# Optimization experiments

Measured on AMD Instinct MI355X. Metric: run time of the kernel, lower is better.

## Reference

```python
import jax, jax.numpy as jnp
import numpy as np


def _ln(x, g, b, eps=1e-5):
    m = x.mean(-1, keepdims=True)
    v = ((x - m) ** 2).mean(-1, keepdims=True)
    return (x - m) / jnp.sqrt(v + eps) * g + b


def _gat_layer(x, src, dst, W, a_src, a_dst, bias, heads, out_ch, concat):
    # PyG GATConv: linear -> per-edge leaky_relu attention -> segment softmax over dst -> scatter-sum
    N = x.shape[0]
    h = (x @ W).reshape(N, heads, out_ch)            # [N,H,C]
    asrc = (h * a_src).sum(-1)                        # [N,H]
    adst = (h * a_dst).sum(-1)                        # [N,H]
    e = jax.nn.leaky_relu(asrc[src] + adst[dst], 0.2)  # [E,H]
    m = jax.ops.segment_max(e, dst, num_segments=N)
    p = jnp.exp(e - m[dst])
    denom = jax.ops.segment_sum(p, dst, num_segments=N)
    alpha = p / (denom[dst] + 1e-16)                  # [E,H]
    out = jax.ops.segment_sum(h[src] * alpha[:, :, None], dst, num_segments=N)  # [N,H,C]
    out = out.reshape(N, heads * out_ch) if concat else out.mean(1)
    return out + bias


def setup_inputs() -> dict:
    k = jax.random.key(0)
    def rn(i, shape, s=0.05):
        return jax.random.normal(jax.random.fold_in(k, i), shape, dtype=jnp.float32) * s
    N, E, B, S = 50000, 800000, 8, 512
    return dict(
        hidden_states=rn(0, (B, S, 768), 1.0),
        attention_mask=jnp.ones((B, S), jnp.int32),
        concept_embeddings_bert=rn(1, (111, 768), 1.0),
        graph_x=rn(2, (N, 256), 1.0),
        edge_index=jax.random.randint(jax.random.fold_in(k, 3), (2, E), 0, N),
        concept_node_idx=jax.random.randint(jax.random.fold_in(k, 4), (111,), 0, N),
        w1=rn(5, (256, 256)), att_src1=rn(6, (4, 64)), att_dst1=rn(7, (4, 64)), bias1=rn(8, (256,)),
        w2=rn(9, (256, 256)), att_src2=rn(10, (1, 256)), att_dst2=rn(11, (1, 256)), bias2=rn(12, (256,)),
        graph_proj_w=rn(13, (768, 256)), graph_proj_b=rn(14, (768,)),
        fusion_w=rn(15, (768, 1536)), fusion_b=rn(16, (768,)),
        fusion_ln_g=jnp.ones((768,), jnp.float32), fusion_ln_b=jnp.zeros((768,), jnp.float32),
        in_proj_w=rn(17, (2304, 768)), in_proj_b=rn(18, (2304,)),
        out_proj_w=rn(19, (768, 768)), out_proj_b=rn(20, (768,)),
        ln_g=jnp.ones((768,), jnp.float32), ln_b=jnp.zeros((768,), jnp.float32),
        concept_head_w=rn(21, (111, 768)), concept_head_b=rn(22, (111,)),
        laat_first_w=rn(23, (768, 768)), laat_second_w=rn(24, (50, 768)),
        laat_output_w=rn(25, (1, 768)), laat_output_b=rn(26, (1,)),
        c2l_w=rn(27, (50, 111)),
        graph_scale=jnp.array([-2.0], jnp.float32),
    )


def reference(hidden_states, attention_mask, concept_embeddings_bert, graph_x, edge_index,
              concept_node_idx, w1, att_src1, att_dst1, bias1, w2, att_src2, att_dst2, bias2,
              graph_proj_w, graph_proj_b, fusion_w, fusion_b, fusion_ln_g, fusion_ln_b,
              in_proj_w, in_proj_b, out_proj_w, out_proj_b, ln_g, ln_b,
              concept_head_w, concept_head_b, laat_first_w, laat_second_w,
              laat_output_w, laat_output_b, c2l_w, graph_scale):
    N = graph_x.shape[0]
    B, S, H = hidden_states.shape
    loop = jnp.arange(N, dtype=edge_index.dtype)  # PyG add_self_loops default
    src = jnp.concatenate([edge_index[0], loop])
    dst = jnp.concatenate([edge_index[1], loop])
    # --- GATEncoder (2 layers, eval mode => dropout identity) ---
    g = _gat_layer(graph_x, src, dst, w1, att_src1, att_dst1, bias1, 4, 64, True)
    g = jax.nn.elu(g)
    g = _gat_layer(g, src, dst, w2, att_src2, att_dst2, bias2, 1, 256, False)  # [N,256]
    gat_concepts = g[concept_node_idx] @ graph_proj_w.T + graph_proj_b          # [NC,768]
    # --- concept fusion ---
    NC = concept_embeddings_bert.shape[0]
    fused_in = jnp.concatenate([
        jnp.broadcast_to(concept_embeddings_bert, (B, NC, H)),
        jnp.broadcast_to(gat_concepts, (B, NC, H))], axis=-1)                   # [B,NC,1536]
    enhanced = jax.nn.relu(_ln(fused_in @ fusion_w.T + fusion_b, fusion_ln_g, fusion_ln_b))
    # --- cross attention (8 heads, dim 96) ---
    wq, wk, wv = in_proj_w[:768], in_proj_w[768:1536], in_proj_w[1536:]
    bq, bk, bv = in_proj_b[:768], in_proj_b[768:1536], in_proj_b[1536:]
    q = (hidden_states @ wq.T + bq).reshape(B, S, 8, 96)
    kk = (enhanced @ wk.T + bk).reshape(B, NC, 8, 96)
    vv = (enhanced @ wv.T + bv).reshape(B, NC, 8, 96)
    scores = jnp.einsum('bshd,bchd->bhsc', q, kk) / jnp.sqrt(jnp.float32(96.0))
    attn = jax.nn.softmax(scores, axis=-1)                                      # [B,8,S,NC]
    ctx = jnp.einsum('bhsc,bchd->bshd', attn, vv).reshape(B, S, H)
    context = ctx @ out_proj_w.T + out_proj_b
    attn_weights = attn.mean(1)                                                 # [B,S,NC]
    # --- concept head on CLS ---
    concept_logits = hidden_states[:, 0] @ concept_head_w.T + concept_head_b
    concept_scores = jax.nn.sigmoid(concept_logits)
    graph_strength = jax.nn.sigmoid(graph_scale[0])
    enriched = _ln(hidden_states + graph_strength * context, ln_g, ln_b)
    # --- LAAT ---
    U = jnp.tanh(enriched @ laat_first_w.T)
    att = U @ laat_second_w.T                                                   # [B,S,ND]
    att = jnp.where(attention_mask[:, :, None] == 0, -jnp.inf, att)
    w = jax.nn.softmax(att, axis=1)
    label_reps = jnp.einsum('bsl,bsh->blh', w, enriched)                        # [B,ND,H]
    logits = (label_reps @ laat_output_w.T)[..., 0] + laat_output_b[0]
    logits = logits + concept_scores @ c2l_w.T
    return (logits, concept_logits, concept_scores, label_reps, attn_weights, graph_strength)
```

## Files before the change

### kernel.cpp

```cpp
#include <hip/hip_runtime.h>
#include <math.h>
#include <stdint.h>

static constexpr int NN = 50000;
static constexpr int EE = 800000;
static constexpr int ET = EE + NN;
static constexpr int BB = 8;
static constexpr int SS = 512;
static constexpr int HH = 768;
static constexpr int NC = 111;
static constexpr int NL = 50;

#define DINL __device__ __forceinline__

typedef __attribute__((ext_vector_type(8))) short bf16x8;
typedef __attribute__((ext_vector_type(4))) float f32x4;

DINL float wsum(float v){
  #pragma unroll
  for (int m=1;m<64;m<<=1) v += __shfl_xor(v, m);
  return v;
}
DINL float wmax(float v){
  #pragma unroll
  for (int m=1;m<64;m<<=1) v = fmaxf(v, __shfl_xor(v, m));
  return v;
}
DINL float4 wsum4(float4 v){
  #pragma unroll
  for (int m=1;m<64;m<<=1){
    v.x += __shfl_xor(v.x,m); v.y += __shfl_xor(v.y,m);
    v.z += __shfl_xor(v.z,m); v.w += __shfl_xor(v.w,m);
  }
  return v;
}
DINL float4 wmax4(float4 v){
  #pragma unroll
  for (int m=1;m<64;m<<=1){
    v.x=fmaxf(v.x,__shfl_xor(v.x,m)); v.y=fmaxf(v.y,__shfl_xor(v.y,m));
    v.z=fmaxf(v.z,__shfl_xor(v.z,m)); v.w=fmaxf(v.w,__shfl_xor(v.w,m));
  }
  return v;
}

__global__ void count_deg_k(const int* __restrict__ eidx, int* __restrict__ deg){
  int i = blockIdx.x*256 + threadIdx.x;
  if (i>=ET) return;
  int d = (i<EE)? eidx[EE + i] : (i - EE);
  atomicAdd(&deg[d], 1);
}

__global__ __launch_bounds__(1024) void scan1_k(const int* __restrict__ deg,
                                                int* __restrict__ incl, int* __restrict__ csum){
  __shared__ int sh[1024];
  int tid = threadIdx.x;
  int i = blockIdx.x*1024 + tid;
  int v = (i<NN)? deg[i] : 0;
  sh[tid] = v;
  __syncthreads();
  for (int off=1; off<1024; off<<=1){
    int t = (tid>=off)? sh[tid-off] : 0;
    __syncthreads();
    sh[tid] += t;
    __syncthreads();
  }
  if (i<NN) incl[i] = sh[tid];
  if (tid==1023) csum[blockIdx.x] = sh[1023];
}

__global__ void scan2_k(int* __restrict__ csum, int nch){
  if (threadIdx.x==0 && blockIdx.x==0){
    int run = 0;
    for (int i=0;i<nch;i++){ int v = csum[i]; csum[i] = run; run += v; }
  }
}

__global__ void scan3_k(const int* __restrict__ deg, const int* __restrict__ incl,
                        const int* __restrict__ csum, int* __restrict__ rowstart){
  int i = blockIdx.x*256 + threadIdx.x;
  if (i>=NN) return;
  int ex = csum[i>>10] + incl[i] - deg[i];
  rowstart[i] = ex;
  if (i==NN-1) rowstart[NN] = ex + deg[i];
}

__global__ void fill_csr_k(const int* __restrict__ eidx, const int* __restrict__ rowstart,
                           int* __restrict__ cursor, int* __restrict__ csr_src, int* __restrict__ csr_dst){
  int i = blockIdx.x*256 + threadIdx.x;
  if (i>=ET) return;
  int s, d;
  if (i<EE){ s = eidx[i]; d = eidx[EE+i]; } else { s = i-EE; d = i-EE; }
  int pos = rowstart[d] + atomicAdd(&cursor[d], 1);
  csr_src[pos] = s; csr_dst[pos] = d;
}

DINL uint bf16_rne(float x){
  uint u = __float_as_uint(x);
  return (u + 0x7FFFu + ((u>>16)&1u)) >> 16;
}
DINL void split8(const float4 v0, const float4 v1, uint4& ph, uint4& pl){
  float xs[8] = {v0.x,v0.y,v0.z,v0.w,v1.x,v1.y,v1.z,v1.w};
  uint hh[8], ll[8];
  #pragma unroll
  for (int i=0;i<8;i++){
    uint hb = bf16_rne(xs[i]);
    float hf = __uint_as_float(hb<<16);
    float lo = xs[i] - hf;
    hh[i] = hb; ll[i] = bf16_rne(lo);
  }
  ph = make_uint4(hh[0]|(hh[1]<<16), hh[2]|(hh[3]<<16), hh[4]|(hh[5]<<16), hh[6]|(hh[7]<<16));
  pl = make_uint4(ll[0]|(ll[1]<<16), ll[2]|(ll[3]<<16), ll[4]|(ll[5]<<16), ll[6]|(ll[7]<<16));
}

__global__ void split_k(const float* __restrict__ in, ushort* __restrict__ hi,
                        ushort* __restrict__ lo, int n){
  int i = blockIdx.x*256 + threadIdx.x;
  if (i>=n) return;
  float x = in[i];
  uint hb = bf16_rne(x);
  float hf = __uint_as_float(hb<<16);
  hi[i] = (ushort)hb;
  lo[i] = (ushort)bf16_rne(x - hf);
}

__global__ void split_t_k(const float* __restrict__ in, ushort* __restrict__ hi,
                          ushort* __restrict__ lo, int R, int C){
  int i = blockIdx.x*256 + threadIdx.x;
  if (i>=R*C) return;
  int n = i / R, k = i - n*R;
  float x = in[k*C + n];
  uint hb = bf16_rne(x);
  float hf = __uint_as_float(hb<<16);
  hi[i] = (ushort)hb;
  lo[i] = (ushort)bf16_rne(x - hf);
}

__global__ __launch_bounds__(256) void gemm_mfma3(
    const float* __restrict__ A, const ushort* __restrict__ Bh, const ushort* __restrict__ Bl,
    const float* __restrict__ bias, float* __restrict__ C, ushort* __restrict__ Cb,
    int M, int N, int K, float alpha, int act)
{
  __shared__ __align__(16) ushort As[2][128*64];
  __shared__ __align__(16) ushort Bs[2][64*64];
  const int tid = threadIdx.x;
  const int lane = tid & 63, wid = tid >> 6;
  const int wm = wid >> 1, wn = wid & 1;
  const int m0 = blockIdx.y*128, n0 = blockIdx.x*64;
  f32x4 acc[4][2];
  #pragma unroll
  for (int i=0;i<4;i++)
    #pragma unroll
    for (int j=0;j<2;j++) acc[i][j] = (f32x4){0.f,0.f,0.f,0.f};

  const int nkt = K >> 6;
  for (int kt=0; kt<nkt; ++kt){
    #pragma unroll
    for (int q=0;q<4;q++){
      int idx = q*256 + tid;
      int row = idx >> 3;
      int g8  = idx & 7;
      int rowg = m0 + row; if (rowg >= M) rowg = M-1;
      const float* src = A + (int64_t)rowg*K + (kt<<6) + g8*8;
      float4 v0 = ((const float4*)src)[0];
      float4 v1 = ((const float4*)src)[1];
      uint4 ph, pl;
      split8(v0, v1, ph, pl);
      int off = row*64 + ((g8*8) ^ ((row&7)<<3));
      *(uint4*)&As[0][off] = ph;
      *(uint4*)&As[1][off] = pl;
    }
    #pragma unroll
    for (int q=0;q<4;q++){
      int idx = q*256 + tid;
      int plane = idx >> 9;
      int rem = idx & 511;
      int row = rem >> 3;
      int g8 = rem & 7;
      const ushort* src = (plane ? Bl : Bh) + (int64_t)(n0+row)*K + (kt<<6) + g8*8;
      uint4 v = *(const uint4*)src;
      int off = row*64 + ((g8*8) ^ ((row&7)<<3));
      *(uint4*)&Bs[plane][off] = v;
    }
    __syncthreads();
    #pragma unroll
    for (int ks=0; ks<2; ks++){
      const int kswz = ks*32 + ((lane>>4)<<3);
      bf16x8 ah[4], al[4], bh[2], bl[2];
      #pragma unroll
      for (int mi=0;mi<4;mi++){
        int r = wm*64 + mi*16 + (lane&15);
        int off = r*64 + (kswz ^ ((r&7)<<3));
        ah[mi] = *(const bf16x8*)&As[0][off];
        al[mi] = *(const bf16x8*)&As[1][off];
      }
      #pragma unroll
      for (int nj=0;nj<2;nj++){
        int r = wn*32 + nj*16 + (lane&15);
        int off = r*64 + (kswz ^ ((r&7)<<3));
        bh[nj] = *(const bf16x8*)&Bs[0][off];
        bl[nj] = *(const bf16x8*)&Bs[1][off];
      }
      #pragma unroll
      for (int mi=0;mi<4;mi++)
        #pragma unroll
        for (int nj=0;nj<2;nj++){
          acc[mi][nj] = __builtin_amdgcn_mfma_f32_16x16x32_bf16(ah[mi], bh[nj], acc[mi][nj], 0,0,0);
          acc[mi][nj] = __builtin_amdgcn_mfma_f32_16x16x32_bf16(ah[mi], bl[nj], acc[mi][nj], 0,0,0);
          acc[mi][nj] = __builtin_amdgcn_mfma_f32_16x16x32_bf16(al[mi], bh[nj], acc[mi][nj], 0,0,0);
        }
    }
    __syncthreads();
  }
  const int crow = (lane>>4)*4, ccol = lane&15;
  #pragma unroll
  for (int nj=0;nj<2;nj++){
    int n = n0 + wn*32 + nj*16 + ccol;
    float bv = bias ? bias[n] : 0.f;
    #pragma unroll
    for (int mi=0;mi<4;mi++){
      #pragma unroll
      for (int j=0;j<4;j++){
        int m = m0 + wm*64 + mi*16 + crow + j;
        if (m < M){
          float v = acc[mi][nj][j]*alpha + bv;
          if (act==1) v = tanhf(v);
          C[(int64_t)m*N + n] = v;
          if (Cb) Cb[(int64_t)m*N + n] = (ushort)bf16_rne(v);
        }
      }
    }
  }
}

template<bool TB>
__global__ __launch_bounds__(256) void gemm_f32(
    const float* __restrict__ A, const float* __restrict__ Bm,
    const float* __restrict__ bias, float* __restrict__ C,
    int M, int N, int K, int lda, int ldb, int ldc,
    int nb2,
    int64_t sA1, int64_t sA2, int64_t sB1, int64_t sB2, int64_t sC1, int64_t sC2,
    float alpha, int act)
{
  int z = blockIdx.z;
  int z1 = z / nb2, z2 = z - z1*nb2;
  A  += z1*sA1 + z2*sA2;
  Bm += z1*sB1 + z2*sB2;
  C  += z1*sC1 + z2*sC2;
  __shared__ __align__(16) float sA[16][132];
  __shared__ __align__(16) float sB[16][68];
  const int tid = threadIdx.x;
  const int m0 = blockIdx.y*128, n0 = blockIdx.x*64;
  const int tx = tid & 15, ty = tid >> 4;
  float acc[8][4] = {};
  for (int k0=0; k0<K; k0+=16){
    {
      int kk = tid & 15, mm = tid >> 4;
      #pragma unroll
      for (int r=0;r<8;r++){
        int m = m0 + mm + r*16, k = k0 + kk;
        float v = 0.f;
        if (m<M && k<K) v = A[(int64_t)m*lda + k];
        sA[kk][mm + r*16] = v;
      }
    }
    if (!TB){
      int nn = tid & 63, kb = tid >> 6;
      #pragma unroll
      for (int r=0;r<4;r++){
        int k = k0 + kb + r*4, n = n0 + nn;
        float v=0.f;
        if (k<K && n<N) v = Bm[(int64_t)k*ldb + n];
        sB[kb + r*4][nn] = v;
      }
    } else {
      int kk = tid & 15, nn = tid >> 4;
      #pragma unroll
      for (int r=0;r<4;r++){
        int n = n0 + nn + r*16, k = k0 + kk;
        float v=0.f;
        if (n<N && k<K) v = Bm[(int64_t)n*ldb + k];
        sB[kk][nn + r*16] = v;
      }
    }
    __syncthreads();
    #pragma unroll
    for (int k=0;k<16;k++){
      float4 a0 = *(const float4*)&sA[k][ty*8];
      float4 a1 = *(const float4*)&sA[k][ty*8+4];
      float4 b  = *(const float4*)&sB[k][tx*4];
      float av[8] = {a0.x,a0.y,a0.z,a0.w,a1.x,a1.y,a1.z,a1.w};
      float bv[4] = {b.x,b.y,b.z,b.w};
      #pragma unroll
      for (int i=0;i<8;i++)
        #pragma unroll
        for (int j=0;j<4;j++)
          acc[i][j] += av[i]*bv[j];
    }
    __syncthreads();
  }
  #pragma unroll
  for (int i=0;i<8;i++){
    int m = m0 + ty*8 + i;
    if (m>=M) continue;
    #pragma unroll
    for (int j=0;j<4;j++){
      int n = n0 + tx*4 + j;
      if (n>=N) continue;
      float v = acc[i][j]*alpha;
      if (bias) v += bias[n];
      if (act==1) v = tanhf(v);
      C[(int64_t)m*ldc + n] = v;
    }
  }
}

__global__ __launch_bounds__(256) void skinny_tb_k(
    const float* __restrict__ A, const float* __restrict__ B,
    const float* __restrict__ bias, float* __restrict__ C,
    int M, int N, int K, int lda, int ldb, int ldc)
{
  int ngroups = (N+3)>>2;
  int w = blockIdx.x*4 + (threadIdx.x>>6);
  if (w >= M*ngroups) return;
  int lane = threadIdx.x & 63;
  int m = w / ngroups, ng = w - m*ngroups;
  int n0 = ng*4;
  const float4* a4 = (const float4*)(A + (int64_t)m*lda);
  int r0 = n0, r1 = (n0+1<N)? n0+1 : N-1, r2 = (n0+2<N)? n0+2 : N-1, r3 = (n0+3<N)? n0+3 : N-1;
  const float4* b0 = (const float4*)(B + (int64_t)r0*ldb);
  const float4* b1 = (const float4*)(B + (int64_t)r1*ldb);
  const float4* b2 = (const float4*)(B + (int64_t)r2*ldb);
  const float4* b3 = (const float4*)(B + (int64_t)r3*ldb);
  float4 acc = make_float4(0.f,0.f,0.f,0.f);
  int K4 = K>>2;
  for (int i=lane; i<K4; i+=64){
    float4 av = a4[i];
    float4 v0 = b0[i], v1 = b1[i], v2 = b2[i], v3 = b3[i];
    acc.x += av.x*v0.x + av.y*v0.y + av.z*v0.z + av.w*v0.w;
    acc.y += av.x*v1.x + av.y*v1.y + av.z*v1.z + av.w*v1.w;
    acc.z += av.x*v2.x + av.y*v2.y + av.z*v2.z + av.w*v2.w;
    acc.w += av.x*v3.x + av.y*v3.y + av.z*v3.z + av.w*v3.w;
  }
  acc = wsum4(acc);
  if (lane==0){
    float vals[4] = {acc.x, acc.y, acc.z, acc.w};
    #pragma unroll
    for (int j=0;j<4;j++){
      int n = n0+j;
      if (n<N){
        float v = vals[j];
        if (bias) v += bias[n];
        C[(int64_t)m*ldc + n] = v;
      }
    }
  }
}

__global__ __launch_bounds__(256) void attcoef1_k(const float* __restrict__ h,
    const float* __restrict__ a_src, const float* __restrict__ a_dst,
    float* __restrict__ asrc, float* __restrict__ adst){
  int node = blockIdx.x*4 + (threadIdx.x>>6);
  if (node>=NN) return;
  int lane = threadIdx.x & 63;
  float4 hv = ((const float4*)h)[(int64_t)node*64 + lane];
  int head = lane >> 4;
  float4 as = ((const float4*)a_src)[head*16 + (lane&15)];
  float4 ad = ((const float4*)a_dst)[head*16 + (lane&15)];
  float ps = hv.x*as.x + hv.y*as.y + hv.z*as.z + hv.w*as.w;
  float pd = hv.x*ad.x + hv.y*ad.y + hv.z*ad.z + hv.w*ad.w;
  #pragma unroll
  for (int m=1;m<16;m<<=1){ ps += __shfl_xor(ps,m); pd += __shfl_xor(pd,m); }
  if ((lane&15)==0){ asrc[node*4+head]=ps; adst[node*4+head]=pd; }
}

__global__ __launch_bounds__(256) void attcoef2_k(const float* __restrict__ h,
    const float* __restrict__ a_src, const float* __restrict__ a_dst,
    float* __restrict__ asrc, float* __restrict__ adst){
  int node = blockIdx.x*4 + (threadIdx.x>>6);
  if (node>=NN) return;
  int lane = threadIdx.x & 63;
  float4 hv = ((const float4*)h)[(int64_t)node*64 + lane];
  float4 as = ((const float4*)a_src)[lane];
  float4 ad = ((const float4*)a_dst)[lane];
  float ps = hv.x*as.x + hv.y*as.y + hv.z*as.z + hv.w*as.w;
  float pd = hv.x*ad.x + hv.y*ad.y + hv.z*ad.z + hv.w*ad.w;
  ps = wsum(ps); pd = wsum(pd);
  if (lane==0){ asrc[node]=ps; adst[node]=pd; }
}

__global__ void edge_e1_k(const int* __restrict__ csr_src, const int* __restrict__ csr_dst,
                          const float* __restrict__ asrc, const float* __restrict__ adst,
                          float* __restrict__ ebuf){
  int p = blockIdx.x*256 + threadIdx.x;
  if (p>=ET) return;
  int s = csr_src[p], d = csr_dst[p];
  float4 a = ((const float4*)asrc)[s];
  float4 b = ((const float4*)adst)[d];
  float4 e;
  e.x = a.x+b.x; e.x = (e.x>=0.f)? e.x : 0.2f*e.x;
  e.y = a.y+b.y; e.y = (e.y>=0.f)? e.y : 0.2f*e.y;
  e.z = a.z+b.z; e.z = (e.z>=0.f)? e.z : 0.2f*e.z;
  e.w = a.w+b.w; e.w = (e.w>=0.f)? e.w : 0.2f*e.w;
  ((float4*)ebuf)[p] = e;
}

__global__ void edge_e2_k(const int* __restrict__ csr_src, const int* __restrict__ csr_dst,
                          const float* __restrict__ asrc, const float* __restrict__ adst,
                          float* __restrict__ ebuf){
  int p = blockIdx.x*256 + threadIdx.x;
  if (p>=ET) return;
  int s = csr_src[p], d = csr_dst[p];
  float e = asrc[s] + adst[d];
  e = (e>=0.f)? e : 0.2f*e;
  ebuf[p] = e;
}

__global__ __launch_bounds__(256) void agg1_k(const ushort* __restrict__ hb, const float* __restrict__ ebuf,
    const int* __restrict__ rowstart, const int* __restrict__ csr_src,
    const float* __restrict__ bias, float* __restrict__ outp){
  int node = blockIdx.x*4 + (threadIdx.x>>6);
  if (node>=NN) return;
  int lane = threadIdx.x & 63;
  int rs = rowstart[node], re = rowstart[node+1];
  const float4* e4 = (const float4*)ebuf;
  float4 mx = make_float4(-INFINITY,-INFINITY,-INFINITY,-INFINITY);
  for (int p=rs+lane; p<re; p+=64){
    float4 e = e4[p];
    mx.x=fmaxf(mx.x,e.x); mx.y=fmaxf(mx.y,e.y); mx.z=fmaxf(mx.z,e.z); mx.w=fmaxf(mx.w,e.w);
  }
  mx = wmax4(mx);
  float4 sm = make_float4(0.f,0.f,0.f,0.f);
  for (int p=rs+lane; p<re; p+=64){
    float4 e = e4[p];
    sm.x += expf(e.x-mx.x); sm.y += expf(e.y-mx.y);
    sm.z += expf(e.z-mx.z); sm.w += expf(e.w-mx.w);
  }
  sm = wsum4(sm);
  int head = lane>>4;
  float m_h = head==0?mx.x:head==1?mx.y:head==2?mx.z:mx.w;
  float s_h = head==0?sm.x:head==1?sm.y:head==2?sm.z:sm.w;
  float dinv = 1.f/(s_h+1e-16f);
  const ushort4* h4 = (const ushort4*)hb;
  float4 acc = make_float4(0.f,0.f,0.f,0.f);
  for (int p=rs; p<re; ++p){
    int s = csr_src[p];
    float w = expf(ebuf[p*4+head]-m_h)*dinv;
    ushort4 hu = h4[(int64_t)s*64 + lane];
    acc.x += w*__uint_as_float(((uint)hu.x)<<16);
    acc.y += w*__uint_as_float(((uint)hu.y)<<16);
    acc.z += w*__uint_as_float(((uint)hu.z)<<16);
    acc.w += w*__uint_as_float(((uint)hu.w)<<16);
  }
  float4 bb = ((const float4*)bias)[lane];
  float4 o;
  o.x = acc.x+bb.x; o.x = (o.x>0.f)? o.x : expm1f(o.x);
  o.y = acc.y+bb.y; o.y = (o.y>0.f)? o.y : expm1f(o.y);
  o.z = acc.z+bb.z; o.z = (o.z>0.f)? o.z : expm1f(o.z);
  o.w = acc.w+bb.w; o.w = (o.w>0.f)? o.w : expm1f(o.w);
  ((float4*)outp)[(int64_t)node*64 + lane] = o;
}

__global__ __launch_bounds__(256) void agg2_k(const ushort* __restrict__ hb, const float* __restrict__ ebuf,
    const int* __restrict__ rowstart, const int* __restrict__ csr_src,
    const float* __restrict__ bias, float* __restrict__ outp){
  int node = blockIdx.x*4 + (threadIdx.x>>6);
  if (node>=NN) return;
  int lane = threadIdx.x & 63;
  int rs = rowstart[node], re = rowstart[node+1];
  float mx = -INFINITY;
  for (int p=rs+lane; p<re; p+=64) mx = fmaxf(mx, ebuf[p]);
  mx = wmax(mx);
  float sm = 0.f;
  for (int p=rs+lane; p<re; p+=64) sm += expf(ebuf[p]-mx);
  sm = wsum(sm);
  float dinv = 1.f/(sm+1e-16f);
  const ushort4* h4 = (const ushort4*)hb;
  float4 acc = make_float4(0.f,0.f,0.f,0.f);
  for (int p=rs; p<re; ++p){
    int s = csr_src[p];
    float w = expf(ebuf[p]-mx)*dinv;
    ushort4 hu = h4[(int64_t)s*64 + lane];
    acc.x += w*__uint_as_float(((uint)hu.x)<<16);
    acc.y += w*__uint_as_float(((uint)hu.y)<<16);
    acc.z += w*__uint_as_float(((uint)hu.z)<<16);
    acc.w += w*__uint_as_float(((uint)hu.w)<<16);
  }
  float4 bb = ((const float4*)bias)[lane];
  float4 o = make_float4(acc.x+bb.x, acc.y+bb.y, acc.z+bb.z, acc.w+bb.w);
  ((float4*)outp)[(int64_t)node*64 + lane] = o;
}

__global__ void gather_gsel_k(const float* __restrict__ out2, const int* __restrict__ cidx,
                              float* __restrict__ gsel){
  int idx = blockIdx.x*256 + threadIdx.x;
  if (idx >= NC*256) return;
  int i = idx >> 8, c = idx & 255;
  gsel[idx] = out2[(int64_t)cidx[i]*256 + c];
}

__global__ void build_fused_k(const float* __restrict__ bert, const float* __restrict__ gatc,
                              float* __restrict__ fused){
  int idx = blockIdx.x*256 + threadIdx.x;
  if (idx >= NC*1536) return;
  int i = idx / 1536, c = idx - i*1536;
  fused[idx] = (c<768)? bert[(int64_t)i*768 + c] : gatc[(int64_t)i*768 + (c-768)];
}

__global__ __launch_bounds__(256) void ln_k(const float* __restrict__ x1, const float* __restrict__ x2,
    const float* __restrict__ gsptr, const float* __restrict__ g, const float* __restrict__ bb,
    float* __restrict__ outp, int relu){
  __shared__ float red[4];
  int row = blockIdx.x;
  int t = threadIdx.x;
  float gs = 0.f;
  if (x2) gs = 1.f/(1.f+expf(-gsptr[0]));
  const float* xr = x1 + (int64_t)row*768;
  float v0 = xr[t], v1 = xr[t+256], v2 = xr[t+512];
  if (x2){
    const float* x2r = x2 + (int64_t)row*768;
    v0 += gs*x2r[t]; v1 += gs*x2r[t+256]; v2 += gs*x2r[t+512];
  }
  int lane = t&63, wid = t>>6;
  float s = wsum(v0+v1+v2);
  if (lane==0) red[wid]=s;
  __syncthreads();
  float mean = (red[0]+red[1]+red[2]+red[3]) * (1.f/768.f);
  __syncthreads();
  float d0=v0-mean, d1=v1-mean, d2=v2-mean;
  float ss = wsum(d0*d0+d1*d1+d2*d2);
  if (lane==0) red[wid]=ss;
  __syncthreads();
  float var = (red[0]+red[1]+red[2]+red[3]) * (1.f/768.f);
  float rstd = rsqrtf(var + 1e-5f);
  float o0 = d0*rstd*g[t]+bb[t];
  float o1 = d1*rstd*g[t+256]+bb[t+256];
  float o2 = d2*rstd*g[t+512]+bb[t+512];
  if (relu){ o0=fmaxf(o0,0.f); o1=fmaxf(o1,0.f); o2=fmaxf(o2,0.f); }
  float* orow = outp + (int64_t)row*768;
  orow[t]=o0; orow[t+256]=o1; orow[t+512]=o2;
}

__global__ __launch_bounds__(256) void softmax_nc_k(float* __restrict__ sc, int rows){
  int row = blockIdx.x*4 + (threadIdx.x>>6);
  if (row>=rows) return;
  int lane = threadIdx.x & 63;
  float* r = sc + (int64_t)row*NC;
  float x0 = r[lane];
  float x1 = (lane+64<NC)? r[lane+64] : -INFINITY;
  float m = wmax(fmaxf(x0,x1));
  float p0 = expf(x0-m);
  float p1 = (lane+64<NC)? expf(x1-m) : 0.f;
  float s = wsum(p0+p1);
  float dinv = 1.f/s;
  r[lane] = p0*dinv;
  if (lane+64<NC) r[lane+64] = p1*dinv;
}

__global__ void mean_heads_k(const float* __restrict__ attn, float* __restrict__ outp){
  int64_t idx = (int64_t)blockIdx.x*256 + threadIdx.x;
  if (idx >= (int64_t)BB*SS*NC) return;
  int c = idx % NC;
  int64_t r = idx / NC;
  int s = r % SS;
  int b = r / SS;
  float acc = 0.f;
  #pragma unroll
  for (int h=0;h<8;h++)
    acc += attn[(((int64_t)(b*8+h)*SS)+s)*NC + c];
  outp[idx] = acc * 0.125f;
}

__global__ void sigmoid_k(const float* __restrict__ in, float* __restrict__ outp, int n,
                          const float* __restrict__ gsptr, float* __restrict__ gsout){
  int idx = blockIdx.x*256 + threadIdx.x;
  if (idx < n) outp[idx] = 1.f/(1.f+expf(-in[idx]));
  if (idx == 0) gsout[0] = 1.f/(1.f+expf(-gsptr[0]));
}

__global__ __launch_bounds__(256) void laat_softmax_k(float* __restrict__ att, const int* __restrict__ mask){
  int idx = blockIdx.x*4 + (threadIdx.x>>6);
  if (idx >= BB*NL) return;
  int lane = threadIdx.x & 63;
  int b = idx / NL, l = idx - b*NL;
  float x[8];
  #pragma unroll
  for (int i=0;i<8;i++){
    int s = lane + i*64;
    int mk = mask[b*SS + s];
    x[i] = mk ? att[((int64_t)(b*SS+s))*NL + l] : -INFINITY;
  }
  float m = -INFINITY;
  #pragma unroll
  for (int i=0;i<8;i++) m = fmaxf(m, x[i]);
  m = wmax(m);
  float p[8]; float sm = 0.f;
  #pragma unroll
  for (int i=0;i<8;i++){ p[i] = expf(x[i]-m); sm += p[i]; }
  sm = wsum(sm);
  float dinv = 1.f/sm;
  #pragma unroll
  for (int i=0;i<8;i++){
    int s = lane + i*64;
    att[((int64_t)(b*SS+s))*NL + l] = p[i]*dinv;
  }
}

__global__ __launch_bounds__(256) void label_reps_k(const float* __restrict__ w,
    const float* __restrict__ enr, float* __restrict__ outp){
  __shared__ __align__(16) float part[4][768];
  int bl = blockIdx.x;
  int b = bl / NL, l = bl - b*NL;
  int t = threadIdx.x;
  int wid = t>>6, lane = t&63;
  const float* wb = w + (int64_t)b*SS*NL + l;
  const float* eb = enr + (int64_t)b*SS*768;
  float4 a0 = make_float4(0,0,0,0), a1 = a0, a2 = a0;
  for (int s=wid; s<SS; s+=4){
    float wv = wb[(int64_t)s*NL];
    const float4* row = (const float4*)(eb + (int64_t)s*768);
    float4 r0 = row[lane], r1 = row[lane+64], r2 = row[lane+128];
    a0.x += wv*r0.x; a0.y += wv*r0.y; a0.z += wv*r0.z; a0.w += wv*r0.w;
    a1.x += wv*r1.x; a1.y += wv*r1.y; a1.z += wv*r1.z; a1.w += wv*r1.w;
    a2.x += wv*r2.x; a2.y += wv*r2.y; a2.z += wv*r2.z; a2.w += wv*r2.w;
  }
  ((float4*)&part[wid][lane*4      ])[0] = a0;
  ((float4*)&part[wid][lane*4 + 256])[0] = a1;
  ((float4*)&part[wid][lane*4 + 512])[0] = a2;
  __syncthreads();
  float* o = outp + (int64_t)bl*768;
  #pragma unroll
  for (int q=0;q<3;q++){
    int ch = t + q*256;
    o[ch] = part[0][ch] + part[1][ch] + part[2][ch] + part[3][ch];
  }
}

__global__ __launch_bounds__(256) void logits_k(const float* __restrict__ lr,
    const float* __restrict__ low, const float* __restrict__ lob,
    const float* __restrict__ cs, const float* __restrict__ c2l,
    float* __restrict__ logits){
  int idx = blockIdx.x*4 + (threadIdx.x>>6);
  if (idx >= BB*NL) return;
  int lane = threadIdx.x & 63;
  int b = idx / NL, l = idx - b*NL;
  const float* r = lr + (int64_t)idx*768;
  float acc = 0.f;
  for (int c=lane;c<768;c+=64) acc += r[c]*low[c];
  for (int c=lane;c<NC;c+=64)  acc += cs[b*NC+c]*c2l[l*NC+c];
  acc = wsum(acc);
  if (lane==0) logits[idx] = acc + lob[0];
}

extern "C" void kernel_launch(void* const* d_in, const int* in_sizes, int n_in,
                              void* d_out, int out_size, void* d_ws, size_t ws_size,
                              hipStream_t stream)
{
  const float* hs    = (const float*)d_in[0];
  const int*   amask = (const int*)d_in[1];
  const float* bert  = (const float*)d_in[2];
  const float* gx    = (const float*)d_in[3];
  const int*   eidx  = (const int*)d_in[4];
  const int*   cidx  = (const int*)d_in[5];
  const float* w1    = (const float*)d_in[6];
  const float* as1   = (const float*)d_in[7];
  const float* ad1   = (const float*)d_in[8];
  const float* b1    = (const float*)d_in[9];
  const float* w2    = (const float*)d_in[10];
  const float* as2   = (const float*)d_in[11];
  const float* ad2   = (const float*)d_in[12];
  const float* b2    = (const float*)d_in[13];
  const float* gpw   = (const float*)d_in[14];
  const float* gpb   = (const float*)d_in[15];
  const float* fw    = (const float*)d_in[16];
  const float* fb    = (const float*)d_in[17];
  const float* flng  = (const float*)d_in[18];
  const float* flnb  = (const float*)d_in[19];
  const float* ipw   = (const float*)d_in[20];
  const float* ipb   = (const float*)d_in[21];
  const float* opw   = (const float*)d_in[22];
  const float* opb   = (const float*)d_in[23];
  const float* lng   = (const float*)d_in[24];
  const float* lnb   = (const float*)d_in[25];
  const float* chw   = (const float*)d_in[26];
  const float* chb   = (const float*)d_in[27];
  const float* lfw   = (const float*)d_in[28];
  const float* lsw   = (const float*)d_in[29];
  const float* low   = (const float*)d_in[30];
  const float* lob   = (const float*)d_in[31];
  const float* c2l   = (const float*)d_in[32];
  const float* gsc   = (const float*)d_in[33];
  float* out = (float*)d_out;

  int* deg      = (int*)d_ws;
  int* cursor   = deg + NN;
  int* rowstart = cursor + NN;
  int* csr_src  = rowstart + (NN+1);
  int* csr_dst  = csr_src + ET;
  int* incl     = csr_dst + ET;
  int* csum     = incl + NN;
  size_t iw = (size_t)NN*2 + (size_t)(NN+1) + (size_t)ET*2 + (size_t)NN + 64;
  float* fbase = (float*)d_ws + ((iw+3) & ~(size_t)3);
  float* ebuf  = fbase;
  float* asrcb = ebuf  + (size_t)ET*4;
  float* adstb = asrcb + (size_t)NN*4;
  float* bufA  = adstb + (size_t)NN*4;
  float* bufB  = bufA  + (size_t)NN*256;
  float* gselb = bufB  + (size_t)NN*256;
  float* gatc  = gselb + (size_t)NC*256;
  float* fusedb= gatc  + (size_t)NC*HH;
  float* kvb   = fusedb+ (size_t)NC*1536;
  float* enhb  = kvb   + (size_t)NC*1536;
  ushort* Wth  = (ushort*)(enhb + (size_t)NC*HH);
  ushort* Wtl  = Wth + 256*256;
  ushort* Wdh  = Wtl + 256*256;
  ushort* Wdl  = Wdh + 768*768;
  ushort* hbb  = Wdl + 768*768;
  float* qb    = bufA;
  float* scb   = bufA + (size_t)BB*SS*HH;
  float* ctxb  = scb  + (size_t)BB*8*SS*NC;
  float* ctxt  = bufB;
  float* enrb  = bufB + (size_t)BB*SS*HH;
  float* Ub    = enrb + (size_t)BB*SS*HH;
  float* attb  = Ub   + (size_t)BB*SS*HH;

  float* out_logits = out;
  float* out_cl = out + 400;
  float* out_cs = out + 1288;
  float* out_lr = out + 2176;
  float* out_aw = out + 309376;
  float* out_gs = out + 764032;

  hipMemsetAsync(deg,    0, sizeof(int)*NN, stream);
  hipMemsetAsync(cursor, 0, sizeof(int)*NN, stream);

  count_deg_k<<<(ET+255)/256,256,0,stream>>>(eidx, deg);
  int nch = (NN+1023)/1024;
  scan1_k<<<nch,1024,0,stream>>>(deg, incl, csum);
  scan2_k<<<1,64,0,stream>>>(csum, nch);
  scan3_k<<<(NN+255)/256,256,0,stream>>>(deg, incl, csum, rowstart);
  fill_csr_k<<<(ET+255)/256,256,0,stream>>>(eidx, rowstart, cursor, csr_src, csr_dst);

  auto gemm = [&](bool tb, const float* A, const float* Bm, const float* bias, float* C,
                  int M, int Nn, int K, int lda, int ldb, int ldc,
                  int nb, int nb2,
                  int64_t sA1,int64_t sA2,int64_t sB1,int64_t sB2,int64_t sC1,int64_t sC2,
                  float alpha, int act){
    dim3 g((Nn+63)/64, (M+127)/128, nb);
    if (tb) gemm_f32<true ><<<g,256,0,stream>>>(A,Bm,bias,C,M,Nn,K,lda,ldb,ldc,nb2,sA1,sA2,sB1,sB2,sC1,sC2,alpha,act);
    else    gemm_f32<false><<<g,256,0,stream>>>(A,Bm,bias,C,M,Nn,K,lda,ldb,ldc,nb2,sA1,sA2,sB1,sB2,sC1,sC2,alpha,act);
  };
  auto skinny = [&](const float* A, const float* Bm, const float* bias, float* C,
                    int M, int Nn, int K, int lda, int ldb, int ldc){
    int ngroups = (Nn+3)>>2;
    int waves = M*ngroups;
    skinny_tb_k<<<(waves+3)/4,256,0,stream>>>(A,Bm,bias,C,M,Nn,K,lda,ldb,ldc);
  };
  auto mfma = [&](const float* A, const ushort* Bh2, const ushort* Bl2, const float* bias,
                  float* C, ushort* Cb, int M, int Nn, int K, float alpha, int act){
    dim3 g(Nn/64, (M+127)/128);
    gemm_mfma3<<<g,256,0,stream>>>(A, Bh2, Bl2, bias, C, Cb, M, Nn, K, alpha, act);
  };

  split_t_k<<<(256*256+255)/256,256,0,stream>>>(w1, Wth, Wtl, 256, 256);
  mfma(gx, Wth, Wtl, nullptr, bufA, hbb, NN, 256, 256, 1.f, 0);
  attcoef1_k<<<(NN+3)/4,256,0,stream>>>(bufA, as1, ad1, asrcb, adstb);
  edge_e1_k<<<(ET+255)/256,256,0,stream>>>(csr_src, csr_dst, asrcb, adstb, ebuf);
  agg1_k<<<(NN+3)/4,256,0,stream>>>(hbb, ebuf, rowstart, csr_src, b1, bufB);
  split_t_k<<<(256*256+255)/256,256,0,stream>>>(w2, Wth, Wtl, 256, 256);
  mfma(bufB, Wth, Wtl, nullptr, bufA, hbb, NN, 256, 256, 1.f, 0);
  attcoef2_k<<<(NN+3)/4,256,0,stream>>>(bufA, as2, ad2, asrcb, adstb);
  edge_e2_k<<<(ET+255)/256,256,0,stream>>>(csr_src, csr_dst, asrcb, adstb, ebuf);
  agg2_k<<<(NN+3)/4,256,0,stream>>>(hbb, ebuf, rowstart, csr_src, b2, bufB);
  gather_gsel_k<<<(NC*256+255)/256,256,0,stream>>>(bufB, cidx, gselb);
  skinny(gselb, gpw, gpb, gatc, NC, HH, 256, 256,256,HH);
  build_fused_k<<<(NC*1536+255)/256,256,0,stream>>>(bert, gatc, fusedb);
  skinny(fusedb, fw, fb, enhb, NC, HH, 1536, 1536,1536,HH);
  ln_k<<<NC,256,0,stream>>>(enhb, nullptr, nullptr, flng, flnb, enhb, 1);
  skinny(enhb, ipw + (size_t)768*768, ipb+768, kvb, NC, 1536, 768, 768,768,1536);
  split_k<<<(768*768+255)/256,256,0,stream>>>(ipw, Wdh, Wdl, 768*768);
  mfma(hs, Wdh, Wdl, ipb, qb, nullptr, BB*SS, HH, HH, 1.f, 0);
  gemm(true, qb, kvb, nullptr, scb, SS, NC, 96, 768, 1536, NC, BB*8, 8,
       (int64_t)SS*HH, 96, 0, 96, (int64_t)8*SS*NC, (int64_t)SS*NC, 0.10206207261596577f, 0);
  softmax_nc_k<<<(BB*8*SS)/4,256,0,stream>>>(scb, BB*8*SS);
  mean_heads_k<<<(int)(((int64_t)BB*SS*NC+255)/256),256,0,stream>>>(scb, out_aw);
  gemm(false, scb, kvb+768, nullptr, ctxb, SS, 96, NC, NC, 1536, HH, BB*8, 8,
       (int64_t)8*SS*NC, (int64_t)SS*NC, 0, 96, (int64_t)SS*HH, 96, 1.f, 0);
  split_k<<<(768*768+255)/256,256,0,stream>>>(opw, Wdh, Wdl, 768*768);
  mfma(ctxb, Wdh, Wdl, opb, ctxt, nullptr, BB*SS, HH, HH, 1.f, 0);
  skinny(hs, chw, chb, out_cl, BB, NC, HH, SS*HH, 768, NC);
  sigmoid_k<<<4,256,0,stream>>>(out_cl, out_cs, BB*NC, gsc, out_gs);
  ln_k<<<BB*SS,256,0,stream>>>(hs, ctxt, gsc, lng, lnb, enrb, 0);
  split_k<<<(768*768+255)/256,256,0,stream>>>(lfw, Wdh, Wdl, 768*768);
  mfma(enrb, Wdh, Wdl, nullptr, Ub, nullptr, BB*SS, HH, HH, 1.f, 1);
  skinny(Ub, lsw, nullptr, attb, BB*SS, NL, HH, 768,768,NL);
  laat_softmax_k<<<(BB*NL+3)/4,256,0,stream>>>(attb, amask);
  label_reps_k<<<BB*NL,256,0,stream>>>(attb, enrb, out_lr);
  logits_k<<<(BB*NL+3)/4,256,0,stream>>>(out_lr, low, lob, out_cs, c2l, out_logits);
}
```

Measured before the change: 1.130 ms.

## Split GAT softmax into per-node stats and per-edge alpha precompute kernels

Moves the segment max/sum reductions out of the aggregation kernels into separate per-node stats kernels, then normalizes edge scores into attention weights in a per-edge pass. The aggregation loop then reads a precomputed weight instead of doing an exp per edge per lane, which removes redundant exp work across the 64 lanes. In exchange it adds two extra kernel launches per layer and an extra full read/write pass over the edge buffer, and it reuses the asrc/adst buffers as node stat storage.

After: 1.171 ms. 3.6% more time.

```diff
diff --git a/kernel.cpp b/kernel.cpp
--- a/kernel.cpp
+++ b/kernel.cpp
@@ -415,9 +415,8 @@
   ebuf[p] = e;
 }
 
-__global__ __launch_bounds__(256) void agg1_k(const ushort* __restrict__ hb, const float* __restrict__ ebuf,
-    const int* __restrict__ rowstart, const int* __restrict__ csr_src,
-    const float* __restrict__ bias, float* __restrict__ outp){
+__global__ __launch_bounds__(256) void stats1_k(const float* __restrict__ ebuf,
+    const int* __restrict__ rowstart, float* __restrict__ nodem, float* __restrict__ noded){
   int node = blockIdx.x*4 + (threadIdx.x>>6);
   if (node>=NN) return;
   int lane = threadIdx.x & 63;
@@ -436,15 +435,62 @@
     sm.z += expf(e.z-mx.z); sm.w += expf(e.w-mx.w);
   }
   sm = wsum4(sm);
+  if (lane==0){
+    ((float4*)nodem)[node] = mx;
+    ((float4*)noded)[node] = make_float4(1.f/(sm.x+1e-16f), 1.f/(sm.y+1e-16f),
+                                         1.f/(sm.z+1e-16f), 1.f/(sm.w+1e-16f));
+  }
+}
+
+__global__ void alpha1_k(float* __restrict__ ebuf, const int* __restrict__ csr_dst,
+                         const float* __restrict__ nodem, const float* __restrict__ noded){
+  int p = blockIdx.x*256 + threadIdx.x;
+  if (p>=ET) return;
+  int d = csr_dst[p];
+  float4 e = ((const float4*)ebuf)[p];
+  float4 m = ((const float4*)nodem)[d];
+  float4 di = ((const float4*)noded)[d];
+  e.x = expf(e.x-m.x)*di.x; e.y = expf(e.y-m.y)*di.y;
+  e.z = expf(e.z-m.z)*di.z; e.w = expf(e.w-m.w)*di.w;
+  ((float4*)ebuf)[p] = e;
+}
+
+__global__ __launch_bounds__(256) void stats2_k(const float* __restrict__ ebuf,
+    const int* __restrict__ rowstart, float* __restrict__ nodem, float* __restrict__ noded){
+  int node = blockIdx.x*4 + (threadIdx.x>>6);
+  if (node>=NN) return;
+  int lane = threadIdx.x & 63;
+  int rs = rowstart[node], re = rowstart[node+1];
+  float mx = -INFINITY;
+  for (int p=rs+lane; p<re; p+=64) mx = fmaxf(mx, ebuf[p]);
+  mx = wmax(mx);
+  float sm = 0.f;
+  for (int p=rs+lane; p<re; p+=64) sm += expf(ebuf[p]-mx);
+  sm = wsum(sm);
+  if (lane==0){ nodem[node]=mx; noded[node]=1.f/(sm+1e-16f); }
+}
+
+__global__ void alpha2_k(float* __restrict__ ebuf, const int* __restrict__ csr_dst,
+                         const float* __restrict__ nodem, const float* __restrict__ noded){
+  int p = blockIdx.x*256 + threadIdx.x;
+  if (p>=ET) return;
+  int d = csr_dst[p];
+  ebuf[p] = expf(ebuf[p]-nodem[d])*noded[d];
+}
+
+__global__ __launch_bounds__(256) void agg1_k(const ushort* __restrict__ hb, const float* __restrict__ ebuf,
+    const int* __restrict__ rowstart, const int* __restrict__ csr_src,
+    const float* __restrict__ bias, float* __restrict__ outp){
+  int node = blockIdx.x*4 + (threadIdx.x>>6);
+  if (node>=NN) return;
+  int lane = threadIdx.x & 63;
+  int rs = rowstart[node], re = rowstart[node+1];
   int head = lane>>4;
-  float m_h = head==0?mx.x:head==1?mx.y:head==2?mx.z:mx.w;
-  float s_h = head==0?sm.x:head==1?sm.y:head==2?sm.z:sm.w;
-  float dinv = 1.f/(s_h+1e-16f);
   const ushort4* h4 = (const ushort4*)hb;
   float4 acc = make_float4(0.f,0.f,0.f,0.f);
   for (int p=rs; p<re; ++p){
     int s = csr_src[p];
-    float w = expf(ebuf[p*4+head]-m_h)*dinv;
+    float w = ebuf[p*4+head];
     ushort4 hu = h4[(int64_t)s*64 + lane];
     acc.x += w*__uint_as_float(((uint)hu.x)<<16);
     acc.y += w*__uint_as_float(((uint)hu.y)<<16);
@@ -467,18 +513,11 @@
   if (node>=NN) return;
   int lane = threadIdx.x & 63;
   int rs = rowstart[node], re = rowstart[node+1];
-  float mx = -INFINITY;
-  for (int p=rs+lane; p<re; p+=64) mx = fmaxf(mx, ebuf[p]);
-  mx = wmax(mx);
-  float sm = 0.f;
-  for (int p=rs+lane; p<re; p+=64) sm += expf(ebuf[p]-mx);
-  sm = wsum(sm);
-  float dinv = 1.f/(sm+1e-16f);
   const ushort4* h4 = (const ushort4*)hb;
   float4 acc = make_float4(0.f,0.f,0.f,0.f);
   for (int p=rs; p<re; ++p){
     int s = csr_src[p];
-    float w = expf(ebuf[p]-mx)*dinv;
+    float w = ebuf[p];
     ushort4 hu = h4[(int64_t)s*64 + lane];
     acc.x += w*__uint_as_float(((uint)hu.x)<<16);
     acc.y += w*__uint_as_float(((uint)hu.y)<<16);
@@ -765,11 +804,15 @@
   mfma(gx, Wth, Wtl, nullptr, bufA, hbb, NN, 256, 256, 1.f, 0);
   attcoef1_k<<<(NN+3)/4,256,0,stream>>>(bufA, as1, ad1, asrcb, adstb);
   edge_e1_k<<<(ET+255)/256,256,0,stream>>>(csr_src, csr_dst, asrcb, adstb, ebuf);
+  stats1_k<<<(NN+3)/4,256,0,stream>>>(ebuf, rowstart, asrcb, adstb);
+  alpha1_k<<<(ET+255)/256,256,0,stream>>>(ebuf, csr_dst, asrcb, adstb);
   agg1_k<<<(NN+3)/4,256,0,stream>>>(hbb, ebuf, rowstart, csr_src, b1, bufB);
   split_t_k<<<(256*256+255)/256,256,0,stream>>>(w2, Wth, Wtl, 256, 256);
   mfma(bufB, Wth, Wtl, nullptr, bufA, hbb, NN, 256, 256, 1.f, 0);
   attcoef2_k<<<(NN+3)/4,256,0,stream>>>(bufA, as2, ad2, asrcb, adstb);
   edge_e2_k<<<(ET+255)/256,256,0,stream>>>(csr_src, csr_dst, asrcb, adstb, ebuf);
+  stats2_k<<<(NN+3)/4,256,0,stream>>>(ebuf, rowstart, asrcb, adstb);
+  alpha2_k<<<(ET+255)/256,256,0,stream>>>(ebuf, csr_dst, asrcb, adstb);
   agg2_k<<<(NN+3)/4,256,0,stream>>>(hbb, ebuf, rowstart, csr_src, b2, bufB);
   gather_gsel_k<<<(NC*256+255)/256,256,0,stream>>>(bufB, cidx, gselb);
   skinny(gselb, gpw, gpb, gatc, NC, HH, 256, 256,256,HH);
```
